# Performance work log

Measured on AMD Instinct MI355X. Metric: run time of the kernel, lower is better.

Reference implementation:

```python
import jax, jax.numpy as jnp
import numpy as np

DIM = 1024
N_HEADS = 16
HEAD_DIM = DIM // N_HEADS
B, S = 2, 2048


def setup_inputs() -> dict:
    key = jax.random.key(0)
    ks = jax.random.split(key, 6)
    scale = 0.02
    return {
        "x": jax.random.normal(ks[0], (B, S, DIM), dtype=jnp.float32),
        "mask": jnp.zeros((1, 1, S, S), dtype=jnp.float32),
        "attn_bias": jax.random.normal(ks[1], (B, N_HEADS, S, S), dtype=jnp.float32),
        "wq": jax.random.normal(ks[2], (DIM, DIM), dtype=jnp.float32) * scale,
        "wk": jax.random.normal(ks[3], (DIM, DIM), dtype=jnp.float32) * scale,
        "wv": jax.random.normal(ks[4], (DIM, DIM), dtype=jnp.float32) * scale,
        "wo": jax.random.normal(ks[5], (DIM, DIM), dtype=jnp.float32) * scale,
    }


def reference(x, mask, attn_bias, wq, wk, wv, wo):
    bsz, seqlen, _ = x.shape
    # nn.Linear(bias=False): y = x @ W.T where W is [out, in]
    xq = (x @ wq.T).reshape(bsz, seqlen, N_HEADS, HEAD_DIM)
    xk = (x @ wk.T).reshape(bsz, seqlen, N_HEADS, HEAD_DIM)
    xv = (x @ wv.T).reshape(bsz, seqlen, N_HEADS, HEAD_DIM)
    # scores: [B, H, S, S]
    scores = jnp.einsum("bqhd,bkhd->bhqk", xq, xk) / np.sqrt(HEAD_DIM).astype(np.float32)
    scores = scores + attn_bias + mask
    probs = jax.nn.softmax(scores.astype(jnp.float32), axis=-1).astype(xq.dtype)
    out = jnp.einsum("bhqk,bkhd->bqhd", probs, xv).reshape(bsz, seqlen, -1)
    return out @ wo.T
```

## Files before the change

### kernel.cpp

```cpp
#include <hip/hip_runtime.h>
#include <hip/hip_bf16.h>

#define BSZ 2
#define SEQ 2048
#define NH 16
#define HD 64
#define DIM 1024
#define MROWS (BSZ*SEQ)

typedef short v8s __attribute__((ext_vector_type(8)));
typedef float v4f __attribute__((ext_vector_type(4)));

__device__ __forceinline__ ushort f2b(float f) {
    unsigned int u = __float_as_uint(f);
    unsigned int r = (u + 0x7fffu + ((u >> 16) & 1u)) >> 16;
    return (ushort)r;
}

__device__ __forceinline__ unsigned pk2(float lo, float hi) {
    unsigned r;
    asm("v_cvt_pk_bf16_f32 %0, %1, %2" : "=v"(r) : "v"(lo), "v"(hi));
    return r;
}

__device__ __forceinline__ void gld16(const void* g, void* l) {
    __builtin_amdgcn_global_load_lds((const __attribute__((address_space(1))) void*)g,
                                     (__attribute__((address_space(3))) void*)l, 16, 0, 0);
}

__global__ void castx(const float* __restrict__ s, ushort* __restrict__ d, int n) {
    int i = (blockIdx.x * 256 + threadIdx.x) * 4;
    if (i < n) {
        float4 v = *reinterpret_cast<const float4*>(s + i);
        ushort4 o;
        o.x = f2b(v.x); o.y = f2b(v.y); o.z = f2b(v.z); o.w = f2b(v.w);
        *reinterpret_cast<ushort4*>(d + i) = o;
    }
}

__global__ void castw(const float* __restrict__ wq, const float* __restrict__ wk,
                      const float* __restrict__ wv, const float* __restrict__ wo,
                      ushort* __restrict__ dst) {
    int i = (blockIdx.x * 256 + threadIdx.x) * 4;
    const float* s; int off;
    if (i < (1 << 20))      { s = wq; off = 0; }
    else if (i < (2 << 20)) { s = wk; off = 1 << 20; }
    else if (i < (3 << 20)) { s = wv; off = 2 << 20; }
    else                    { s = wo; off = 3 << 20; }
    float4 v = *reinterpret_cast<const float4*>(s + (i - off));
    ushort4 o;
    o.x = f2b(v.x); o.y = f2b(v.y); o.z = f2b(v.z); o.w = f2b(v.w);
    *reinterpret_cast<ushort4*>(dst + i) = o;
}

template<int MODE>
__global__ __launch_bounds__(256) void gemm128(const ushort* __restrict__ A,
                                               const ushort* __restrict__ Bw,
                                               ushort* __restrict__ oq,
                                               ushort* __restrict__ ok,
                                               ushort* __restrict__ ov,
                                               float* __restrict__ of) {
    __shared__ __align__(16) ushort As[128 * 64];
    __shared__ __align__(16) ushort Bs[128 * 64];
    const int bm = blockIdx.x, bn = blockIdx.y;
    const int t = threadIdx.x;
    const int w = t >> 6, l = t & 63;
    const int g = l >> 4, lr = l & 15;
    const int wr = w >> 1, wc = w & 1;

    v4f acc[4][4];
    #pragma unroll
    for (int i = 0; i < 4; i++)
        #pragma unroll
        for (int j = 0; j < 4; j++) acc[i][j] = (v4f){0.f, 0.f, 0.f, 0.f};

    for (int kt = 0; kt < 16; ++kt) {
        const int k0 = kt * 64;
        __syncthreads();
        #pragma unroll
        for (int i = 0; i < 4; ++i) {
            int c = i * 256 + t;
            int row = c >> 3;
            int cc  = (c & 7) ^ (row & 7);
            gld16(A  + (size_t)(bm * 128 + row) * 1024 + k0 + cc * 8,
                  (ushort*)As + (i * 256 + w * 64) * 8);
            gld16(Bw + (size_t)(bn * 128 + row) * 1024 + k0 + cc * 8,
                  (ushort*)Bs + (i * 256 + w * 64) * 8);
        }
        __syncthreads();
        #pragma unroll
        for (int ks = 0; ks < 64; ks += 32) {
            v8s af[4], bf[4];
            #pragma unroll
            for (int i = 0; i < 4; i++) {
                int ar = wr * 64 + i * 16 + lr;
                int br = wc * 64 + i * 16 + lr;
                int ch = ((ks >> 3) + g) ^ (lr & 7);
                af[i] = *reinterpret_cast<const v8s*>(&As[ar * 64 + ch * 8]);
                bf[i] = *reinterpret_cast<const v8s*>(&Bs[br * 64 + ch * 8]);
            }
            #pragma unroll
            for (int i = 0; i < 4; i++)
                #pragma unroll
                for (int j = 0; j < 4; j++)
                    acc[i][j] = __builtin_amdgcn_mfma_f32_16x16x32_bf16(af[i], bf[j], acc[i][j], 0, 0, 0);
        }
    }

    if (MODE == 0) {
        const int region = bn >> 3;
        const float scale = (region == 0) ? 0.125f : 1.0f;
        #pragma unroll
        for (int i = 0; i < 4; i++) {
            int m0 = bm * 128 + wr * 64 + i * 16 + g * 4;
            #pragma unroll
            for (int j = 0; j < 4; j++) {
                int nl = (bn & 7) * 128 + wc * 64 + j * 16 + lr;
                if (region == 2) {
                    int bb = m0 >> 11, s0 = m0 & 2047;
                    int hh = nl >> 6, dd = nl & 63;
                    ushort4 o4;
                    o4.x = f2b(acc[i][j][0]); o4.y = f2b(acc[i][j][1]);
                    o4.z = f2b(acc[i][j][2]); o4.w = f2b(acc[i][j][3]);
                    *reinterpret_cast<ushort4*>(&ov[((size_t)(bb * NH + hh) * HD + dd) * SEQ + s0]) = o4;
                } else {
                    ushort* dst = (region == 0) ? oq : ok;
                    #pragma unroll
                    for (int r = 0; r < 4; r++)
                        dst[(size_t)(m0 + r) * 1024 + nl] = f2b(acc[i][j][r] * scale);
                }
            }
        }
    } else {
        #pragma unroll
        for (int i = 0; i < 4; i++) {
            int m0 = bm * 128 + wr * 64 + i * 16 + g * 4;
            #pragma unroll
            for (int j = 0; j < 4; j++) {
                int n = bn * 128 + wc * 64 + j * 16 + lr;
                #pragma unroll
                for (int r = 0; r < 4; r++)
                    of[(size_t)(m0 + r) * 1024 + n] = acc[i][j][r];
            }
        }
    }
}

__global__ __launch_bounds__(256, 2) void attn_kernel(const ushort* __restrict__ Q,
                                                      const ushort* __restrict__ Kb,
                                                      const ushort* __restrict__ Vt,
                                                      const float* __restrict__ bias,
                                                      ushort* __restrict__ O) {
    __shared__ __align__(16) ushort Ks[2][64 * 64];
    __shared__ __align__(16) ushort Vs[2][64 * 64];
    __shared__ __align__(16) float  Bf[2][64 * 64];
    __shared__ __align__(16) ushort Ps[4][16 * 64];

    const int bh = blockIdx.x, qblk = blockIdx.y;
    const int b = bh >> 4, h = bh & 15;
    const int t = threadIdx.x, w = t >> 6, l = t & 63;
    const int lr = l & 15, g = l >> 4;
    const int L = lr & 7;
    const int qg = qblk * 64 + w * 16 + lr;
    const int rot = (qblk + bh * 5) & 31;

    v8s qf[2];
    #pragma unroll
    for (int d0 = 0; d0 < 2; ++d0)
        qf[d0] = *reinterpret_cast<const v8s*>(&Q[((size_t)(b * SEQ + qg) * NH + h) * HD + d0 * 32 + g * 8]);
    asm volatile("s_waitcnt vmcnt(0)" ::: "memory");
    __builtin_amdgcn_sched_barrier(0);

    float m_run = -1e30f, l_run = 0.f;
    v4f oacc[4];
    #pragma unroll
    for (int dt = 0; dt < 4; ++dt) oacc[dt] = (v4f){0.f, 0.f, 0.f, 0.f};

    const ushort* kbase = Kb + ((size_t)b * SEQ * NH + h) * HD;
    const ushort* vbase = Vt + (size_t)bh * HD * SEQ;
    const float*  bbase = bias + (size_t)bh * SEQ * SEQ + (size_t)(qblk * 64) * SEQ;

    const int srow = t >> 3;
    const int ssw  = (t & 7) ^ (srow & 7);
    const int brow = w * 4 + g;
    const int bsw  = lr ^ (brow & 7);

    auto stage = [&](int buf, int kp) {
        const int k0 = kp * 64;
        #pragma unroll
        for (int c = 0; c < 2; ++c) {
            int row = srow + c * 32;
            gld16(kbase + (size_t)(k0 + row) * (NH * HD) + ssw * 8,
                  (ushort*)Ks[buf] + (c * 256 + w * 64) * 8);
            gld16(vbase + (size_t)row * SEQ + k0 + ssw * 8,
                  (ushort*)Vs[buf] + (c * 256 + w * 64) * 8);
        }
        #pragma unroll
        for (int c = 0; c < 4; ++c) {
            int row = c * 16 + brow;
            gld16(bbase + (size_t)row * SEQ + k0 + bsw * 4,
                  (float*)Bf[buf] + (c * 256 + w * 64) * 4);
        }
    };

    stage(0, rot);
    stage(1, (1 + rot) & 31);

    #pragma unroll 1
    for (int kt = 0; kt < 32; ++kt) {
        const int cur = kt & 1;

        if (kt < 31) asm volatile("s_waitcnt vmcnt(8)" ::: "memory");
        else         asm volatile("s_waitcnt vmcnt(0)" ::: "memory");
        __builtin_amdgcn_sched_barrier(0);
        __builtin_amdgcn_s_barrier();
        __builtin_amdgcn_sched_barrier(0);

        v4f sacc[4];
        #pragma unroll
        for (int nt = 0; nt < 4; ++nt) sacc[nt] = (v4f){0.f, 0.f, 0.f, 0.f};
        __builtin_amdgcn_s_setprio(1);
        #pragma unroll
        for (int nt = 0; nt < 4; ++nt) {
            #pragma unroll
            for (int d0 = 0; d0 < 2; ++d0) {
                v8s kf = *reinterpret_cast<const v8s*>(
                    &Ks[cur][(nt * 16 + lr) * 64 + (((d0 * 4 + g) ^ L) * 8)]);
                sacc[nt] = __builtin_amdgcn_mfma_f32_16x16x32_bf16(kf, qf[d0], sacc[nt], 0, 0, 0);
            }
        }
        __builtin_amdgcn_s_setprio(0);

        float mx = -1e30f;
        #pragma unroll
        for (int nt = 0; nt < 4; ++nt) {
            v4f br = *reinterpret_cast<const v4f*>(
                &Bf[cur][(w * 16 + lr) * 64 + (((nt * 4 + g) ^ L) * 4)]);
            sacc[nt] += br;
            mx = fmaxf(mx, fmaxf(fmaxf(sacc[nt][0], sacc[nt][1]), fmaxf(sacc[nt][2], sacc[nt][3])));
        }
        mx = fmaxf(mx, __shfl_xor(mx, 16));
        mx = fmaxf(mx, __shfl_xor(mx, 32));
        float mnew = fmaxf(m_run, mx);
        float corr = __expf(m_run - mnew);
        m_run = mnew;
        float rs = 0.f;
        #pragma unroll
        for (int nt = 0; nt < 4; ++nt)
            #pragma unroll
            for (int r = 0; r < 4; ++r) {
                float e = __expf(sacc[nt][r] - mnew);
                sacc[nt][r] = e;
                rs += e;
            }
        rs += __shfl_xor(rs, 16);
        rs += __shfl_xor(rs, 32);
        l_run = l_run * corr + rs;
        #pragma unroll
        for (int dt = 0; dt < 4; ++dt) oacc[dt] *= corr;

        #pragma unroll
        for (int nt = 0; nt < 4; ++nt) {
            unsigned lo = pk2(sacc[nt][0], sacc[nt][1]);
            unsigned hi = pk2(sacc[nt][2], sacc[nt][3]);
            int idx = lr * 64 + ((nt * 16 + g * 4) ^ (L << 3));
            *reinterpret_cast<unsigned*>(&Ps[w][idx])     = lo;
            *reinterpret_cast<unsigned*>(&Ps[w][idx + 2]) = hi;
        }

        __builtin_amdgcn_s_setprio(1);
        #pragma unroll
        for (int c0 = 0; c0 < 2; ++c0) {
            v8s pf = *reinterpret_cast<const v8s*>(&Ps[w][lr * 64 + (((c0 * 4 + g) ^ L) * 8)]);
            #pragma unroll
            for (int dt = 0; dt < 4; ++dt) {
                v8s vf = *reinterpret_cast<const v8s*>(
                    &Vs[cur][(dt * 16 + lr) * 64 + (((c0 * 4 + g) ^ L) * 8)]);
                oacc[dt] = __builtin_amdgcn_mfma_f32_16x16x32_bf16(vf, pf, oacc[dt], 0, 0, 0);
            }
        }
        __builtin_amdgcn_s_setprio(0);

        __builtin_amdgcn_sched_barrier(0);
        __builtin_amdgcn_s_barrier();
        __builtin_amdgcn_sched_barrier(0);
        if (kt < 30) stage(cur, (kt + 2 + rot) & 31);
    }

    float inv = 1.f / l_run;
    #pragma unroll
    for (int dt = 0; dt < 4; ++dt) {
        ushort4 o4;
        o4.x = f2b(oacc[dt][0] * inv); o4.y = f2b(oacc[dt][1] * inv);
        o4.z = f2b(oacc[dt][2] * inv); o4.w = f2b(oacc[dt][3] * inv);
        *reinterpret_cast<ushort4*>(&O[((size_t)(b * SEQ + qg) * NH + h) * HD + dt * 16 + g * 4]) = o4;
    }
}

extern "C" void kernel_launch(void* const* d_in, const int* in_sizes, int n_in,
                              void* d_out, int out_size, void* d_ws, size_t ws_size,
                              hipStream_t stream) {
    (void)in_sizes; (void)n_in; (void)out_size; (void)ws_size;
    const float* x    = (const float*)d_in[0];
    const float* bias = (const float*)d_in[2];
    const float* wq   = (const float*)d_in[3];
    const float* wk   = (const float*)d_in[4];
    const float* wv   = (const float*)d_in[5];
    const float* wo   = (const float*)d_in[6];
    float* out = (float*)d_out;

    ushort* xb    = (ushort*)d_ws;
    ushort* wcomb = xb    + (4 << 20);
    ushort* qb    = wcomb + (4 << 20);
    ushort* kb    = qb    + (4 << 20);
    ushort* vtb   = kb    + (4 << 20);
    ushort* ob    = vtb   + (4 << 20);

    castx<<<4096, 256, 0, stream>>>(x, xb, 1 << 22);
    castw<<<4096, 256, 0, stream>>>(wq, wk, wv, wo, wcomb);

    gemm128<0><<<dim3(32, 24), 256, 0, stream>>>(xb, wcomb, qb, kb, vtb, nullptr);

    attn_kernel<<<dim3(32, 32), 256, 0, stream>>>(qb, kb, vtb, bias, ob);

    gemm128<1><<<dim3(32, 8), 256, 0, stream>>>(ob, wcomb + (size_t)3072 * 1024,
                                                nullptr, nullptr, nullptr, out);
}
```

Measured before the change: 214.9 us.

## Double attention block to 128 queries and triple-buffer bias tiles

The attention kernel now uses 512-thread blocks covering 128 query rows, so each staged K/V tile is shared by eight waves instead of four, halving K/V global traffic per query. The bias stream, the dominant memory traffic, moves to a three-deep ring buffer in LDS so it is prefetched two iterations ahead, with vmcnt waits adjusted to match. The cost is one block per CU with a larger LDS footprint (about 130KB) and half as many blocks in the grid, which lowers occupancy and may hurt latency hiding.

```diff
diff --git a/kernel.cpp b/kernel.cpp
--- a/kernel.cpp
+++ b/kernel.cpp
@@ -146,22 +146,22 @@
     }
 }
 
-__global__ __launch_bounds__(256, 2) void attn_kernel(const ushort* __restrict__ Q,
+__global__ __launch_bounds__(512, 1) void attn_kernel(const ushort* __restrict__ Q,
                                                       const ushort* __restrict__ Kb,
                                                       const ushort* __restrict__ Vt,
                                                       const float* __restrict__ bias,
                                                       ushort* __restrict__ O) {
     __shared__ __align__(16) ushort Ks[2][64 * 64];
     __shared__ __align__(16) ushort Vs[2][64 * 64];
-    __shared__ __align__(16) float  Bf[2][64 * 64];
-    __shared__ __align__(16) ushort Ps[4][16 * 64];
+    __shared__ __align__(16) float  Bp[3][128 * 64];
+    __shared__ __align__(16) ushort Ps[8][16 * 64];
 
     const int bh = blockIdx.x, qblk = blockIdx.y;
     const int b = bh >> 4, h = bh & 15;
     const int t = threadIdx.x, w = t >> 6, l = t & 63;
     const int lr = l & 15, g = l >> 4;
     const int L = lr & 7;
-    const int qg = qblk * 64 + w * 16 + lr;
+    const int qg = qblk * 128 + w * 16 + lr;
     const int rot = (qblk + bh * 5) & 31;
 
     v8s qf[2];
@@ -178,40 +178,42 @@
 
     const ushort* kbase = Kb + ((size_t)b * SEQ * NH + h) * HD;
     const ushort* vbase = Vt + (size_t)bh * HD * SEQ;
-    const float*  bbase = bias + (size_t)bh * SEQ * SEQ + (size_t)(qblk * 64) * SEQ;
+    const float*  bbase = bias + (size_t)bh * SEQ * SEQ + (size_t)(qblk * 128) * SEQ;
 
     const int srow = t >> 3;
     const int ssw  = (t & 7) ^ (srow & 7);
-    const int brow = w * 4 + g;
-    const int bsw  = lr ^ (brow & 7);
-
-    auto stage = [&](int buf, int kp) {
+    const int brow7 = (t >> 4) & 7;
+    const int bsw   = (t & 15) ^ brow7;
+
+    auto stage_kv = [&](int buf, int kp) {
         const int k0 = kp * 64;
-        #pragma unroll
-        for (int c = 0; c < 2; ++c) {
-            int row = srow + c * 32;
-            gld16(kbase + (size_t)(k0 + row) * (NH * HD) + ssw * 8,
-                  (ushort*)Ks[buf] + (c * 256 + w * 64) * 8);
-            gld16(vbase + (size_t)row * SEQ + k0 + ssw * 8,
-                  (ushort*)Vs[buf] + (c * 256 + w * 64) * 8);
-        }
+        gld16(kbase + (size_t)(k0 + srow) * (NH * HD) + ssw * 8,
+              (ushort*)Ks[buf] + (w * 64) * 8);
+        gld16(vbase + (size_t)srow * SEQ + k0 + ssw * 8,
+              (ushort*)Vs[buf] + (w * 64) * 8);
+    };
+    auto stage_bias = [&](int buf, int kp) {
+        const int k0 = kp * 64;
         #pragma unroll
         for (int c = 0; c < 4; ++c) {
-            int row = c * 16 + brow;
+            int row = c * 32 + (t >> 4);
             gld16(bbase + (size_t)row * SEQ + k0 + bsw * 4,
-                  (float*)Bf[buf] + (c * 256 + w * 64) * 4);
+                  (float*)Bp[buf] + (c * 512 + w * 64) * 4);
         }
     };
 
-    stage(0, rot);
-    stage(1, (1 + rot) & 31);
-
+    stage_kv(0, rot);                 stage_bias(0, rot);
+    stage_kv(1, (1 + rot) & 31);      stage_bias(1, (1 + rot) & 31);
+    stage_bias(2, (2 + rot) & 31);
+
+    int cb = 0;
     #pragma unroll 1
-    for (int kt = 0; kt < 32; ++kt) {
-        const int cur = kt & 1;
-
-        if (kt < 31) asm volatile("s_waitcnt vmcnt(8)" ::: "memory");
-        else         asm volatile("s_waitcnt vmcnt(0)" ::: "memory");
+    for (int j = 0; j < 32; ++j) {
+        const int cur = j & 1;
+
+        if (j < 30)      asm volatile("s_waitcnt vmcnt(10)" ::: "memory");
+        else if (j == 30) asm volatile("s_waitcnt vmcnt(6)" ::: "memory");
+        else             asm volatile("s_waitcnt vmcnt(0)" ::: "memory");
         __builtin_amdgcn_sched_barrier(0);
         __builtin_amdgcn_s_barrier();
         __builtin_amdgcn_sched_barrier(0);
@@ -235,7 +237,7 @@
         #pragma unroll
         for (int nt = 0; nt < 4; ++nt) {
             v4f br = *reinterpret_cast<const v4f*>(
-                &Bf[cur][(w * 16 + lr) * 64 + (((nt * 4 + g) ^ L) * 4)]);
+                &Bp[cb][(w * 16 + lr) * 64 + (((nt * 4 + g) ^ L) * 4)]);
             sacc[nt] += br;
             mx = fmaxf(mx, fmaxf(fmaxf(sacc[nt][0], sacc[nt][1]), fmaxf(sacc[nt][2], sacc[nt][3])));
         }
@@ -284,7 +286,9 @@
         __builtin_amdgcn_sched_barrier(0);
         __builtin_amdgcn_s_barrier();
         __builtin_amdgcn_sched_barrier(0);
-        if (kt < 30) stage(cur, (kt + 2 + rot) & 31);
+        if (j < 30) stage_kv(cur, (j + 2 + rot) & 31);
+        if (j < 29) stage_bias(cb, (j + 3 + rot) & 31);
+        cb = (cb == 2) ? 0 : cb + 1;
     }
 
     float inv = 1.f / l_run;
@@ -321,7 +325,7 @@
 
     gemm128<0><<<dim3(32, 24), 256, 0, stream>>>(xb, wcomb, qb, kb, vtb, nullptr);
 
-    attn_kernel<<<dim3(32, 32), 256, 0, stream>>>(qb, kb, vtb, bias, ob);
+    attn_kernel<<<dim3(32, 16), 512, 0, stream>>>(qb, kb, vtb, bias, ob);
 
     gemm128<1><<<dim3(32, 8), 256, 0, stream>>>(ob, wcomb + (size_t)3072 * 1024,
                                                 nullptr, nullptr, nullptr, out);
```

Result: slower. 227.4 us (+5.8%).
